# Kernel optimization log

Hardware: AMD Instinct MI355X
Metric: run time of the kernel (lower is better)

Reference implementation:

```python
import jax, jax.numpy as jnp
import numpy as np

B, L, E, H = 2, 256, 512, 8
HD = E // H  # 64


def setup_inputs() -> dict:
    key = jax.random.key(0)
    ks = jax.random.split(key, 11)
    w_scale = 0.04  # ~ xavier std for 512x512
    return {
        "query": jax.random.normal(ks[0], (B, L, E), jnp.float32),
        "key": jax.random.normal(ks[1], (B, L, E), jnp.float32),
        "value": jax.random.normal(ks[2], (B, L, E), jnp.float32),
        "relation": jax.random.normal(ks[3], (B, L, L, E), jnp.float32),
        "Wq": jax.random.normal(ks[4], (E, E), jnp.float32) * w_scale,
        "Wk": jax.random.normal(ks[5], (E, E), jnp.float32) * w_scale,
        "Wv": jax.random.normal(ks[6], (E, E), jnp.float32) * w_scale,
        "Wr": jax.random.normal(ks[7], (E, E), jnp.float32) * w_scale,
        "br": jnp.zeros((E,), jnp.float32),
        "Wo": jax.random.normal(ks[8], (E, E), jnp.float32) * w_scale,
        "bo": jnp.zeros((E,), jnp.float32),
    }


def reference(query, key, value, relation, Wq, Wk, Wv, Wr, br, Wo, bo):
    # relation_project: nn.Linear -> x @ W.T + b, (B,L,L,E)
    r = relation @ Wr.T + br
    # source uses right-multiplication by raw parameter matrices,
    # and (faithfully) projects value with the QUERY weight.
    q = query @ Wq    # (B,L,E)
    k = key @ Wk      # (B,L,E)
    v = value @ Wq    # bug preserved from source
    q = q.reshape(B, L, H, HD)
    k = k.reshape(B, L, H, HD)
    v = v.reshape(B, L, H, HD)
    # q broadcast over key positions plus per-pair relation bias: (B,L,L,H,HD)
    qr = q[:, :, None, :, :] + r.reshape(B, L, L, H, HD)
    a = jnp.einsum('bqkhe,bkhe->bqkh', qr, k) / jnp.sqrt(jnp.float32(HD))
    a = jax.nn.softmax(a, axis=2)  # softmax over key positions (dim 2)
    attn = jnp.einsum('bqkh,bkhe->bqhe', a, v).reshape(B, L, E)
    out = attn @ Wo.T + bo  # out_proj
    return out, a
```

## Files before the change

kernel.cpp:

```cpp
#include <hip/hip_runtime.h>

#define DEV_INLINE __device__ __forceinline__

typedef float nfloat4 __attribute__((ext_vector_type(4)));

static constexpr int Bb = 2, Ls = 256, E = 512, H = 8;
static constexpr int BL = Bb * Ls;

static constexpr size_t WS_QP = 0;
static constexpr size_t WS_KP = WS_QP + (size_t)BL * E;
static constexpr size_t WS_VP = WS_KP + (size_t)BL * E;
static constexpr size_t WS_M  = WS_VP + (size_t)BL * E;
static constexpr size_t WS_C  = WS_M  + (size_t)BL * H * E;
static constexpr size_t WS_O  = WS_C  + (size_t)BL * H;

DEV_INLINE float dot4f(float4 a, float4 b) {
  return a.x * b.x + a.y * b.y + a.z * b.z + a.w * b.w;
}
DEV_INLINE float dot4n(nfloat4 a, float4 b) {
  return a.x * b.x + a.y * b.y + a.z * b.z + a.w * b.w;
}

template <int TRANSB>
DEV_INLINE void gemm_tile(const float* __restrict__ A, int lda,
                          const float* __restrict__ B, int ldb,
                          float* __restrict__ C, int ldc, int Ksz,
                          const float* __restrict__ bias) {
  __shared__ float As[16][68];
  __shared__ float Bs[16][68];
  const int t = threadIdx.x;
  const int tx = t & 15, ty = t >> 4;
  const int i0 = blockIdx.y * 64, j0 = blockIdx.x * 64;
  float acc[4][4] = {};
  for (int k0 = 0; k0 < Ksz; k0 += 16) {
    {
      const int ka = t & 15, ia = t >> 4;
#pragma unroll
      for (int r = 0; r < 4; ++r)
        As[ka][ia + 16 * r] = A[(size_t)(i0 + ia + 16 * r) * lda + (k0 + ka)];
    }
    if (TRANSB == 0) {
      const int jb = t & 63, kb = t >> 6;
#pragma unroll
      for (int r = 0; r < 4; ++r)
        Bs[kb + 4 * r][jb] = B[(size_t)(k0 + kb + 4 * r) * ldb + (j0 + jb)];
    } else {
      const int kb = t & 15, jb = t >> 4;
#pragma unroll
      for (int r = 0; r < 4; ++r)
        Bs[kb][jb + 16 * r] = B[(size_t)(j0 + jb + 16 * r) * ldb + (k0 + kb)];
    }
    __syncthreads();
#pragma unroll
    for (int kk = 0; kk < 16; ++kk) {
      float4 a4 = *(const float4*)&As[kk][ty * 4];
      float4 b4 = *(const float4*)&Bs[kk][tx * 4];
      acc[0][0] += a4.x * b4.x; acc[0][1] += a4.x * b4.y;
      acc[0][2] += a4.x * b4.z; acc[0][3] += a4.x * b4.w;
      acc[1][0] += a4.y * b4.x; acc[1][1] += a4.y * b4.y;
      acc[1][2] += a4.y * b4.z; acc[1][3] += a4.y * b4.w;
      acc[2][0] += a4.z * b4.x; acc[2][1] += a4.z * b4.y;
      acc[2][2] += a4.z * b4.z; acc[2][3] += a4.z * b4.w;
      acc[3][0] += a4.w * b4.x; acc[3][1] += a4.w * b4.y;
      acc[3][2] += a4.w * b4.z; acc[3][3] += a4.w * b4.w;
    }
    __syncthreads();
  }
#pragma unroll
  for (int r = 0; r < 4; ++r) {
#pragma unroll
    for (int c2 = 0; c2 < 4; ++c2) {
      float v = acc[r][c2];
      if (bias) v += bias[j0 + tx * 4 + c2];
      C[(size_t)(i0 + ty * 4 + r) * ldc + (j0 + tx * 4 + c2)] = v;
    }
  }
}

__global__ __launch_bounds__(256) void k1_proj(
    const float* __restrict__ q, const float* __restrict__ k,
    const float* __restrict__ v, const float* __restrict__ Wq,
    const float* __restrict__ Wk, float* __restrict__ qp,
    float* __restrict__ kp, float* __restrict__ vp) {
  const float* A; const float* Bm; float* C;
  switch (blockIdx.z) {
    case 0:  A = q; Bm = Wq; C = qp; break;
    case 1:  A = k; Bm = Wk; C = kp; break;
    default: A = v; Bm = Wq; C = vp; break;
  }
  gemm_tile<0>(A, 512, Bm, 512, C, 512, 512, nullptr);
}

__global__ __launch_bounds__(256) void k2_M(const float* __restrict__ kp,
                                            const float* __restrict__ Wr,
                                            const float* __restrict__ br,
                                            float* __restrict__ M,
                                            float* __restrict__ c) {
  const int h = blockIdx.z;
  if (blockIdx.x == 0 && threadIdx.x < 64) {
    const int row = blockIdx.y * 64 + threadIdx.x;
    float s = 0.f;
    const float* kr = kp + (size_t)row * 512 + h * 64;
    const float* bb = br + h * 64;
#pragma unroll 8
    for (int d = 0; d < 64; ++d) s += bb[d] * kr[d];
    c[(size_t)row * 8 + h] = s;
  }
  gemm_tile<0>(kp + h * 64, 512, Wr + (size_t)h * 64 * 512, 512,
               M + (size_t)h * 512, 4096, 64, nullptr);
}

__global__ __launch_bounds__(256) void k4_rel(
    const float* __restrict__ rel, const float* __restrict__ Mw,
    const float* __restrict__ qp, const float* __restrict__ kp,
    const float* __restrict__ cbias, float* __restrict__ logits) {
  const int blk = blockIdx.x;
  const int bk = blk >> 2;
  const int qq = blk & 3;
  const int b = bk >> 8, k = bk & 255;
  const int t = threadIdx.x, w = t >> 6, lane = t & 63;

  const float* Mbase = Mw + (size_t)bk * 8 * 512;
  float4 m0[8], m1[8];
#pragma unroll
  for (int h = 0; h < 8; ++h) {
    m0[h] = *(const float4*)(Mbase + h * 512 + 4 * lane);
    m1[h] = *(const float4*)(Mbase + h * 512 + 256 + 4 * lane);
  }
  const float* kpr = kp + (size_t)(b * 256 + k) * 512;
  float4 kp0 = *(const float4*)(kpr + 4 * lane);
  float4 kp1 = *(const float4*)(kpr + 256 + 4 * lane);

  const int hq = lane >> 4;
  float w0[4];
#pragma unroll
  for (int h = 0; h < 4; ++h) w0[h] = (hq == h) ? 1.f : 0.f;

  const int hw = ((lane & 1) << 2) | (lane & 2) | ((lane >> 2) & 1);
  const float cv = cbias[(size_t)(b * 256 + k) * 8 + hw];

  const int q0 = qq * 64 + w;
  const nfloat4* relp =
      (const nfloat4*)(rel) + (((size_t)b * 256 + q0) * 256 + k) * 128;
  const float4* qpp = (const float4*)(qp) + (size_t)(b * 256 + q0) * 128;
  float* lp = logits + (((size_t)b * 256 + q0) * 256 + k) * 8 + hw;
  const bool writer = (lane < 8);
  const size_t REL_STRIDE = (size_t)4 * 256 * 128;
  const size_t QP_STRIDE = (size_t)4 * 128;
  const size_t L_STRIDE = (size_t)4 * 256 * 8;

  const bool b0 = (lane & 1) != 0;
  const bool b1 = (lane & 2) != 0;
  const bool b2 = (lane & 4) != 0;

  for (int i = 0; i < 16; ++i) {
    nfloat4 r0 = __builtin_nontemporal_load(&relp[lane]);
    nfloat4 r1 = __builtin_nontemporal_load(&relp[64 + lane]);
    float4 qv0 = qpp[lane];
    float4 qv1 = qpp[64 + lane];

    float acc[8];
#pragma unroll
    for (int h = 0; h < 8; ++h)
      acc[h] = dot4n(r0, m0[h]) + dot4n(r1, m1[h]);
    const float qk0 = dot4f(qv0, kp0);
    const float qk1 = dot4f(qv1, kp1);
#pragma unroll
    for (int h = 0; h < 4; ++h) {
      acc[h] += qk0 * w0[h];
      acc[4 + h] += qk1 * w0[h];
    }

    float s[4];
#pragma unroll
    for (int j = 0; j < 4; ++j) {
      float lo = acc[j], hi = acc[j + 4];
      float send = b0 ? lo : hi;
      float keep = b0 ? hi : lo;
      s[j] = keep + __shfl_xor(send, 1);
    }
    float u[2];
#pragma unroll
    for (int j = 0; j < 2; ++j) {
      float lo = s[j], hi = s[j + 2];
      float send = b1 ? lo : hi;
      float keep = b1 ? hi : lo;
      u[j] = keep + __shfl_xor(send, 2);
    }
    {
      float lo = u[0], hi = u[1];
      float send = b2 ? lo : hi;
      float keep = b2 ? hi : lo;
      float v = keep + __shfl_xor(send, 4);
      v += __shfl_xor(v, 8);
      v += __shfl_xor(v, 16);
      v += __shfl_xor(v, 32);
      if (writer) *lp = v + cv;
    }
    relp += REL_STRIDE;
    qpp += QP_STRIDE;
    lp += L_STRIDE;
  }
}

__global__ __launch_bounds__(256) void k5_softmax(float* __restrict__ logits,
                                                  const float* __restrict__ vp,
                                                  float* __restrict__ o) {
  const int bq = blockIdx.x;
  const int b = bq >> 8;
  const int t = threadIdx.x;
  float* L = logits + (size_t)bq * 2048;
  float4 x0 = ((float4*)L)[t * 2];
  float4 x1 = ((float4*)L)[t * 2 + 1];
  float x[8] = {x0.x, x0.y, x0.z, x0.w, x1.x, x1.y, x1.z, x1.w};
  const float SCALE = 0.125f;
#pragma unroll
  for (int j = 0; j < 8; ++j) x[j] *= SCALE;

  __shared__ float tr[8][272];
  __shared__ float mx[8], sm[8];
#pragma unroll
  for (int hh = 0; hh < 8; ++hh) tr[hh][t] = x[hh];
  __syncthreads();
  const int g = t >> 5, j = t & 31;
  float m = -1e30f;
#pragma unroll
  for (int i = 0; i < 8; ++i) m = fmaxf(m, tr[g][j + 32 * i]);
#pragma unroll
  for (int off = 16; off >= 1; off >>= 1) m = fmaxf(m, __shfl_down(m, off, 32));
  if (j == 0) mx[g] = m;
  __syncthreads();
  float p[8];
#pragma unroll
  for (int hh = 0; hh < 8; ++hh) p[hh] = __expf(x[hh] - mx[hh]);
#pragma unroll
  for (int hh = 0; hh < 8; ++hh) tr[hh][t] = p[hh];
  __syncthreads();
  float ss = 0.f;
#pragma unroll
  for (int i = 0; i < 8; ++i) ss += tr[g][j + 32 * i];
#pragma unroll
  for (int off = 16; off >= 1; off >>= 1) ss += __shfl_down(ss, off, 32);
  if (j == 0) sm[g] = ss;
  __syncthreads();
  float inv[8];
#pragma unroll
  for (int hh = 0; hh < 8; ++hh) inv[hh] = 1.0f / sm[hh];
#pragma unroll
  for (int hh = 0; hh < 8; ++hh) x[hh] = p[hh] * inv[hh];
  ((float4*)L)[t * 2] = make_float4(x[0], x[1], x[2], x[3]);
  ((float4*)L)[t * 2 + 1] = make_float4(x[4], x[5], x[6], x[7]);

  const float invh = inv[g];
  const float2* V2 = ((const float2*)(vp + (size_t)b * 256 * 512)) + t;
  float2 acc2; acc2.x = 0.f; acc2.y = 0.f;
#pragma unroll 8
  for (int kk = 0; kk < 256; ++kk) {
    float wgt = tr[g][kk];
    float2 v = V2[(size_t)kk * 256];
    acc2.x += wgt * v.x;
    acc2.y += wgt * v.y;
  }
  acc2.x *= invh;
  acc2.y *= invh;
  ((float2*)(o + (size_t)bq * 512))[t] = acc2;
}

__global__ __launch_bounds__(256) void k6_out(const float* __restrict__ o,
                                              const float* __restrict__ Wo,
                                              const float* __restrict__ bo,
                                              float* __restrict__ out) {
  gemm_tile<1>(o, 512, Wo, 512, out, 512, 512, bo);
}

extern "C" void kernel_launch(void* const* d_in, const int* in_sizes, int n_in,
                              void* d_out, int out_size, void* d_ws,
                              size_t ws_size, hipStream_t stream) {
  const float* query = (const float*)d_in[0];
  const float* key   = (const float*)d_in[1];
  const float* value = (const float*)d_in[2];
  const float* rel   = (const float*)d_in[3];
  const float* Wq    = (const float*)d_in[4];
  const float* Wk    = (const float*)d_in[5];
  const float* Wr    = (const float*)d_in[7];
  const float* br    = (const float*)d_in[8];
  const float* Wo    = (const float*)d_in[9];
  const float* bo    = (const float*)d_in[10];

  float* out = (float*)d_out;
  float* a   = (float*)d_out + (size_t)BL * E;

  float* ws = (float*)d_ws;
  float* qp = ws + WS_QP;
  float* kp = ws + WS_KP;
  float* vp = ws + WS_VP;
  float* M  = ws + WS_M;
  float* c  = ws + WS_C;
  float* o  = ws + WS_O;

  k1_proj<<<dim3(8, 8, 3), 256, 0, stream>>>(query, key, value, Wq, Wk, qp, kp, vp);
  k2_M<<<dim3(8, 8, 8), 256, 0, stream>>>(kp, Wr, br, M, c);
  k4_rel<<<dim3(2048), 256, 0, stream>>>(rel, M, qp, kp, c, a);
  k5_softmax<<<dim3(512), 256, 0, stream>>>(a, vp, o);
  k6_out<<<dim3(8, 8, 1), 256, 0, stream>>>(o, Wo, bo, out);
}
```

Measured before the change: 467.0 us.

## Precompute per-head QK scores as a GEMM and prefetch relation rows in rel kernel

Adds a batched GEMM kernel that computes the per-head q·k scores plus the relation-bias term into a workspace buffer. The relation kernel then reads one scalar instead of recomputing the dot products from the q and k projections in its inner loop. The relation kernel also prefetches the next relation rows one iteration ahead to overlap load latency. The shared GEMM tile loader now uses float4 global loads, and the softmax-times-V stage splits the key range across two thread groups with float4 V loads and a shared-memory reduction. The cost is an extra kernel launch and an extra workspace buffer.

```diff
diff --git a/kernel.cpp b/kernel.cpp
--- a/kernel.cpp
+++ b/kernel.cpp
@@ -13,10 +13,8 @@
 static constexpr size_t WS_M  = WS_VP + (size_t)BL * E;
 static constexpr size_t WS_C  = WS_M  + (size_t)BL * H * E;
 static constexpr size_t WS_O  = WS_C  + (size_t)BL * H;
-
-DEV_INLINE float dot4f(float4 a, float4 b) {
-  return a.x * b.x + a.y * b.y + a.z * b.z + a.w * b.w;
-}
+static constexpr size_t WS_QK = WS_O  + (size_t)BL * E;
+
 DEV_INLINE float dot4n(nfloat4 a, float4 b) {
   return a.x * b.x + a.y * b.y + a.z * b.z + a.w * b.w;
 }
@@ -30,25 +28,26 @@
   __shared__ float Bs[16][68];
   const int t = threadIdx.x;
   const int tx = t & 15, ty = t >> 4;
+  const int ar = t >> 2, ac = t & 3;
   const int i0 = blockIdx.y * 64, j0 = blockIdx.x * 64;
   float acc[4][4] = {};
   for (int k0 = 0; k0 < Ksz; k0 += 16) {
     {
-      const int ka = t & 15, ia = t >> 4;
-#pragma unroll
-      for (int r = 0; r < 4; ++r)
-        As[ka][ia + 16 * r] = A[(size_t)(i0 + ia + 16 * r) * lda + (k0 + ka)];
+      float4 av = *(const float4*)&A[(size_t)(i0 + ar) * lda + (k0 + 4 * ac)];
+      As[4 * ac + 0][ar] = av.x;
+      As[4 * ac + 1][ar] = av.y;
+      As[4 * ac + 2][ar] = av.z;
+      As[4 * ac + 3][ar] = av.w;
     }
     if (TRANSB == 0) {
-      const int jb = t & 63, kb = t >> 6;
-#pragma unroll
-      for (int r = 0; r < 4; ++r)
-        Bs[kb + 4 * r][jb] = B[(size_t)(k0 + kb + 4 * r) * ldb + (j0 + jb)];
+      float4 bv = *(const float4*)&B[(size_t)(k0 + ty) * ldb + (j0 + 4 * tx)];
+      *(float4*)&Bs[ty][4 * tx] = bv;
     } else {
-      const int kb = t & 15, jb = t >> 4;
-#pragma unroll
-      for (int r = 0; r < 4; ++r)
-        Bs[kb][jb + 16 * r] = B[(size_t)(j0 + jb + 16 * r) * ldb + (k0 + kb)];
+      float4 bv = *(const float4*)&B[(size_t)(j0 + ar) * ldb + (k0 + 4 * ac)];
+      Bs[4 * ac + 0][ar] = bv.x;
+      Bs[4 * ac + 1][ar] = bv.y;
+      Bs[4 * ac + 2][ar] = bv.z;
+      Bs[4 * ac + 3][ar] = bv.w;
     }
     __syncthreads();
 #pragma unroll
@@ -104,16 +103,27 @@
     const float* bb = br + h * 64;
 #pragma unroll 8
     for (int d = 0; d < 64; ++d) s += bb[d] * kr[d];
-    c[(size_t)row * 8 + h] = s;
+    c[((size_t)(row >> 8) * 8 + h) * 256 + (row & 255)] = s;
   }
   gemm_tile<0>(kp + h * 64, 512, Wr + (size_t)h * 64 * 512, 512,
                M + (size_t)h * 512, 4096, 64, nullptr);
 }
 
+__global__ __launch_bounds__(256) void k3_qk(const float* __restrict__ qp,
+                                             const float* __restrict__ kp,
+                                             const float* __restrict__ c,
+                                             float* __restrict__ qk) {
+  const int z = blockIdx.z;
+  const int b = z >> 3, h = z & 7;
+  gemm_tile<1>(qp + (size_t)b * 256 * 512 + h * 64, 512,
+               kp + (size_t)b * 256 * 512 + h * 64, 512,
+               qk + (size_t)z * 65536, 256, 64,
+               c + (size_t)z * 256);
+}
+
 __global__ __launch_bounds__(256) void k4_rel(
     const float* __restrict__ rel, const float* __restrict__ Mw,
-    const float* __restrict__ qp, const float* __restrict__ kp,
-    const float* __restrict__ cbias, float* __restrict__ logits) {
+    const float* __restrict__ qk, float* __restrict__ logits) {
   const int blk = blockIdx.x;
   const int bk = blk >> 2;
   const int qq = blk & 3;
@@ -127,49 +137,42 @@
     m0[h] = *(const float4*)(Mbase + h * 512 + 4 * lane);
     m1[h] = *(const float4*)(Mbase + h * 512 + 256 + 4 * lane);
   }
-  const float* kpr = kp + (size_t)(b * 256 + k) * 512;
-  float4 kp0 = *(const float4*)(kpr + 4 * lane);
-  float4 kp1 = *(const float4*)(kpr + 256 + 4 * lane);
-
-  const int hq = lane >> 4;
-  float w0[4];
-#pragma unroll
-  for (int h = 0; h < 4; ++h) w0[h] = (hq == h) ? 1.f : 0.f;
 
   const int hw = ((lane & 1) << 2) | (lane & 2) | ((lane >> 2) & 1);
-  const float cv = cbias[(size_t)(b * 256 + k) * 8 + hw];
 
   const int q0 = qq * 64 + w;
   const nfloat4* relp =
       (const nfloat4*)(rel) + (((size_t)b * 256 + q0) * 256 + k) * 128;
-  const float4* qpp = (const float4*)(qp) + (size_t)(b * 256 + q0) * 128;
+  const float* qkp = qk + ((size_t)(b * 8 + hw) * 256 + q0) * 256 + k;
   float* lp = logits + (((size_t)b * 256 + q0) * 256 + k) * 8 + hw;
   const bool writer = (lane < 8);
   const size_t REL_STRIDE = (size_t)4 * 256 * 128;
-  const size_t QP_STRIDE = (size_t)4 * 128;
+  const size_t QK_STRIDE = (size_t)4 * 256;
   const size_t L_STRIDE = (size_t)4 * 256 * 8;
 
   const bool b0 = (lane & 1) != 0;
   const bool b1 = (lane & 2) != 0;
   const bool b2 = (lane & 4) != 0;
 
+  nfloat4 r0 = __builtin_nontemporal_load(&relp[lane]);
+  nfloat4 r1 = __builtin_nontemporal_load(&relp[64 + lane]);
+
   for (int i = 0; i < 16; ++i) {
-    nfloat4 r0 = __builtin_nontemporal_load(&relp[lane]);
-    nfloat4 r1 = __builtin_nontemporal_load(&relp[64 + lane]);
-    float4 qv0 = qpp[lane];
-    float4 qv1 = qpp[64 + lane];
+    float qkv = 0.f;
+    if (writer) qkv = *qkp;
+
+    const bool more = (i < 15);
+    nfloat4 nr0, nr1;
+    if (more) {
+      relp += REL_STRIDE;
+      nr0 = __builtin_nontemporal_load(&relp[lane]);
+      nr1 = __builtin_nontemporal_load(&relp[64 + lane]);
+    }
 
     float acc[8];
 #pragma unroll
     for (int h = 0; h < 8; ++h)
       acc[h] = dot4n(r0, m0[h]) + dot4n(r1, m1[h]);
-    const float qk0 = dot4f(qv0, kp0);
-    const float qk1 = dot4f(qv1, kp1);
-#pragma unroll
-    for (int h = 0; h < 4; ++h) {
-      acc[h] += qk0 * w0[h];
-      acc[4 + h] += qk1 * w0[h];
-    }
 
     float s[4];
 #pragma unroll
@@ -195,10 +198,10 @@
       v += __shfl_xor(v, 8);
       v += __shfl_xor(v, 16);
       v += __shfl_xor(v, 32);
-      if (writer) *lp = v + cv;
-    }
-    relp += REL_STRIDE;
-    qpp += QP_STRIDE;
+      if (writer) *lp = v + qkv;
+    }
+    if (more) { r0 = nr0; r1 = nr1; }
+    qkp += QK_STRIDE;
     lp += L_STRIDE;
   }
 }
@@ -219,6 +222,7 @@
 
   __shared__ float tr[8][272];
   __shared__ float mx[8], sm[8];
+  __shared__ float ob[512];
 #pragma unroll
   for (int hh = 0; hh < 8; ++hh) tr[hh][t] = x[hh];
   __syncthreads();
@@ -251,19 +255,36 @@
   ((float4*)L)[t * 2] = make_float4(x[0], x[1], x[2], x[3]);
   ((float4*)L)[t * 2 + 1] = make_float4(x[4], x[5], x[6], x[7]);
 
-  const float invh = inv[g];
-  const float2* V2 = ((const float2*)(vp + (size_t)b * 256 * 512)) + t;
-  float2 acc2; acc2.x = 0.f; acc2.y = 0.f;
+  const int g2 = t >> 7, tc = t & 127;
+  const int hc = tc >> 4;
+  const float invh = inv[hc];
+  const float4* V4 =
+      (const float4*)(vp + (size_t)b * 256 * 512 + (size_t)g2 * 128 * 512) + tc;
+  const float* trh = &tr[hc][g2 * 128];
+  float ax = 0.f, ay = 0.f, az = 0.f, aw = 0.f;
 #pragma unroll 8
-  for (int kk = 0; kk < 256; ++kk) {
-    float wgt = tr[g][kk];
-    float2 v = V2[(size_t)kk * 256];
-    acc2.x += wgt * v.x;
-    acc2.y += wgt * v.y;
-  }
-  acc2.x *= invh;
-  acc2.y *= invh;
-  ((float2*)(o + (size_t)bq * 512))[t] = acc2;
+  for (int kk = 0; kk < 128; ++kk) {
+    const float wgt = trh[kk];
+    float4 vv = V4[(size_t)kk * 128];
+    ax += wgt * vv.x;
+    ay += wgt * vv.y;
+    az += wgt * vv.z;
+    aw += wgt * vv.w;
+  }
+  if (g2) {
+    ob[4 * tc + 0] = ax;
+    ob[4 * tc + 1] = ay;
+    ob[4 * tc + 2] = az;
+    ob[4 * tc + 3] = aw;
+  }
+  __syncthreads();
+  if (!g2) {
+    ax = (ax + ob[4 * tc + 0]) * invh;
+    ay = (ay + ob[4 * tc + 1]) * invh;
+    az = (az + ob[4 * tc + 2]) * invh;
+    aw = (aw + ob[4 * tc + 3]) * invh;
+    ((float4*)(o + (size_t)bq * 512))[tc] = make_float4(ax, ay, az, aw);
+  }
 }
 
 __global__ __launch_bounds__(256) void k6_out(const float* __restrict__ o,
@@ -291,16 +312,18 @@
   float* a   = (float*)d_out + (size_t)BL * E;
 
   float* ws = (float*)d_ws;
-  float* qp = ws + WS_QP;
-  float* kp = ws + WS_KP;
-  float* vp = ws + WS_VP;
-  float* M  = ws + WS_M;
-  float* c  = ws + WS_C;
-  float* o  = ws + WS_O;
+  float* qp  = ws + WS_QP;
+  float* kp  = ws + WS_KP;
+  float* vp  = ws + WS_VP;
+  float* M   = ws + WS_M;
+  float* c   = ws + WS_C;
+  float* o   = ws + WS_O;
+  float* qkb = ws + WS_QK;
 
   k1_proj<<<dim3(8, 8, 3), 256, 0, stream>>>(query, key, value, Wq, Wk, qp, kp, vp);
   k2_M<<<dim3(8, 8, 8), 256, 0, stream>>>(kp, Wr, br, M, c);
-  k4_rel<<<dim3(2048), 256, 0, stream>>>(rel, M, qp, kp, c, a);
+  k3_qk<<<dim3(4, 4, 16), 256, 0, stream>>>(qp, kp, c, qkb);
+  k4_rel<<<dim3(2048), 256, 0, stream>>>(rel, M, qkb, a);
   k5_softmax<<<dim3(512), 256, 0, stream>>>(a, vp, o);
   k6_out<<<dim3(8, 8, 1), 256, 0, stream>>>(o, Wo, bo, out);
 }
```

New measurement: 462.8 us. No clear change (-0.9%).
